# Kernel tuning notes

Hardware: AMD Instinct MI355X
Metric: run time of the kernel (lower is better)

The kernel has to match this reference:

```python
import jax, jax.numpy as jnp
import numpy as np
import math

B, S, D_MODEL, H = 4, 256, 2048, 256
HEAD_DIM = D_MODEL // H  # 8


def setup_inputs() -> dict:
    key = jax.random.key(0)
    ks = jax.random.split(key, 10)
    w_scale = 0.02
    inp = {
        "x": jax.random.normal(ks[0], (B, S, D_MODEL), dtype=jnp.float32),
        "phase_shift": jax.random.normal(ks[1], (H, 1, 1), dtype=jnp.float32),
        "Wq": jax.random.normal(ks[2], (D_MODEL, D_MODEL), dtype=jnp.float32) * w_scale,
        "bq": jnp.zeros((D_MODEL,), dtype=jnp.float32),
        "Wk": jax.random.normal(ks[3], (D_MODEL, D_MODEL), dtype=jnp.float32) * w_scale,
        "bk": jnp.zeros((D_MODEL,), dtype=jnp.float32),
        "Wv": jax.random.normal(ks[4], (D_MODEL, D_MODEL), dtype=jnp.float32) * w_scale,
        "bv": jnp.zeros((D_MODEL,), dtype=jnp.float32),
        "Wo": jax.random.normal(ks[5], (D_MODEL, D_MODEL), dtype=jnp.float32) * w_scale,
        "bo": jnp.zeros((D_MODEL,), dtype=jnp.float32),
    }
    return inp


def _forward(x, phase_shift, Wq, bq, Wk, bk, Wv, bv, Wo, bo):
    b, s, dm = x.shape
    h = phase_shift.shape[0]
    d = dm // h
    # projections (torch Linear with random weights; stored as [in,out])
    q = (x @ Wq + bq).reshape(b, s, h, d)
    k = (x @ Wk + bk).reshape(b, s, h, d)
    v = (x @ Wv + bv).reshape(b, s, h, d)
    # complex phase rotation: q *= exp(+i phi), k *= exp(-i phi)
    # phase_shift (h,1,1) broadcasts against (b,s,h,d) -> varies along the s dim (requires s==h)
    c = jnp.cos(phase_shift)  # (h,1,1)
    sn = jnp.sin(phase_shift)
    qr, qi = q * c, q * sn          # Re/Im of rotated q
    kr, ki = k * c, -(k * sn)       # Re/Im of rotated k
    scale = 1.0 / math.sqrt(d)
    # per-(b,s) head-mixing scores: [b,s,h,h], complex matmul split into real/imag
    sr = (jnp.einsum('bshd,bsgd->bshg', qr, kr)
          - jnp.einsum('bshd,bsgd->bshg', qi, ki)) * scale
    si = (jnp.einsum('bshd,bsgd->bshg', qr, ki)
          + jnp.einsum('bshd,bsgd->bshg', qi, kr)) * scale  # analytically 0 (phases cancel)
    attn_r = jax.nn.softmax(sr, axis=-1)
    attn_i = jax.nn.softmax(si, axis=-1)  # faithful dual softmax; v is real so only
    # Re(attention @ v) = attn_r @ v reaches the output (.real is taken before o_proj)
    del attn_i
    out = jnp.einsum('bshg,bsgd->bshd', attn_r, v).reshape(b, s, dm)
    return out @ Wo + bo


def reference(x, phase_shift, Wq, bq, Wk, bk, Wv, bv, Wo, bo):
    return _forward(x, phase_shift, Wq, bq, Wk, bk, Wv, bv, Wo, bo)
```

## Files before the change

kernel.cpp:

```cpp
#include <hip/hip_runtime.h>
#include <math.h>

#define M_TOK 1024
#define DM    2048
#define NH    256
#define HD    8
#define SCALE 0.35355339059327373f
#define LOG2E 1.4426950408889634f

typedef _Float16 f16x8 __attribute__((ext_vector_type(8)));
typedef _Float16 f16x4 __attribute__((ext_vector_type(4)));
typedef float    f32x4 __attribute__((ext_vector_type(4)));

#if defined(__has_builtin)
#  if __has_builtin(__builtin_amdgcn_exp2f)
#    define EXP2(x) __builtin_amdgcn_exp2f(x)
#  endif
#endif
#ifndef EXP2
#  define EXP2(x) exp2f(x)
#endif

template<int N>
__device__ __forceinline__ void vm_wait() {
    if constexpr (N == 0) asm volatile("s_waitcnt vmcnt(0)" ::: "memory");
    else if constexpr (N == 1) asm volatile("s_waitcnt vmcnt(1)" ::: "memory");
    else if constexpr (N == 2) asm volatile("s_waitcnt vmcnt(2)" ::: "memory");
    else if constexpr (N == 3) asm volatile("s_waitcnt vmcnt(3)" ::: "memory");
    else if constexpr (N == 4) asm volatile("s_waitcnt vmcnt(4)" ::: "memory");
    else if constexpr (N == 5) asm volatile("s_waitcnt vmcnt(5)" ::: "memory");
    else if constexpr (N == 6) asm volatile("s_waitcnt vmcnt(6)" ::: "memory");
    else if constexpr (N == 7) asm volatile("s_waitcnt vmcnt(7)" ::: "memory");
    else static_assert(N <= 7, "add vmcnt case");
}

__device__ __forceinline__ void raw_barrier() {
    asm volatile("" ::: "memory");
    __builtin_amdgcn_s_barrier();
    asm volatile("" ::: "memory");
}

__global__ __launch_bounds__(256) void prep(
    const float* __restrict__ x, _Float16* __restrict__ xh,
    const float* __restrict__ W0, const float* __restrict__ W1,
    const float* __restrict__ W2, const float* __restrict__ W3,
    _Float16* __restrict__ T0, _Float16* __restrict__ T1,
    _Float16* __restrict__ T2, _Float16* __restrict__ T3)
{
    __shared__ float t[64][65];
    const int tid = threadIdx.x;
    const int z   = blockIdx.z;

    if (z == 4) {
        const int i = (blockIdx.y * 32 + blockIdx.x) * 256 + tid;
        const float4 a = ((const float4*)x)[2 * i];
        const float4 b = ((const float4*)x)[2 * i + 1];
        f16x8 v;
        v[0] = (_Float16)a.x; v[1] = (_Float16)a.y; v[2] = (_Float16)a.z; v[3] = (_Float16)a.w;
        v[4] = (_Float16)b.x; v[5] = (_Float16)b.y; v[6] = (_Float16)b.z; v[7] = (_Float16)b.w;
        ((f16x8*)xh)[i] = v;
        return;
    }

    const float* W = (z == 0) ? W0 : (z == 1) ? W1 : (z == 2) ? W2 : W3;
    _Float16*    T = (z == 0) ? T0 : (z == 1) ? T1 : (z == 2) ? T2 : T3;

    const int nb = blockIdx.x * 64;
    const int kb = blockIdx.y * 64;
    const int tr = tid >> 4;
    const int tc = (tid & 15) << 2;

    #pragma unroll
    for (int rr = 0; rr < 4; ++rr) {
        const int k = kb + rr * 16 + tr;
        const float4 v = *(const float4*)&W[(size_t)k * DM + nb + tc];
        t[rr * 16 + tr][tc + 0] = v.x;
        t[rr * 16 + tr][tc + 1] = v.y;
        t[rr * 16 + tr][tc + 2] = v.z;
        t[rr * 16 + tr][tc + 3] = v.w;
    }
    __syncthreads();
    #pragma unroll
    for (int rr = 0; rr < 4; ++rr) {
        const int n = nb + rr * 16 + tr;
        f16x4 v;
        #pragma unroll
        for (int j = 0; j < 4; ++j)
            v[j] = (_Float16)t[tc + j][rr * 16 + tr];
        *(f16x4*)&T[(size_t)n * DM + kb + tc] = v;
    }
}

template<int WGR, int WGC, int WTR, int WTC, bool F16OUT, int CS, bool SPLIT>
__global__ __launch_bounds__(512, 2) void gemm_p3(
    const _Float16* __restrict__ A,
    const _Float16* __restrict__ Bt,
    const float* __restrict__ b0, const float* __restrict__ b1,
    const float* __restrict__ b2, void* __restrict__ C)
{
    constexpr int NW  = WGR * WGC;
    static_assert(NW == 8, "8 waves");
    constexpr int BM  = WGR * WTR * 16;
    constexpr int BN  = WGC * WTC * 16;
    constexpr int NA  = BM / 8;
    constexpr int NB  = BN / 8;
    constexpr int NC  = NA + NB;
    constexpr int CPW = NC / NW;
    static_assert(NC % NW == 0);
    constexpr int S0  = (CPW + 1) / 2;
    constexpr int BUF = (BM + BN) * 64;
    constexpr int KT  = 32;
    static_assert((KT - 2) % 3 == 0 || true);

    __shared__ _Float16 smem[3 * BUF];

    const int bn = blockIdx.x * BN;
    const int bm = blockIdx.y * BM;

    const int tid  = threadIdx.x;
    const int lane = tid & 63;
    const int wv   = tid >> 6;
    const int wr   = (wv / WGC) * (WTR * 16);
    const int wc   = (wv % WGC) * (WTC * 16);
    const int lr   = lane & 15;
    const int lk   = lane >> 4;
    const int rx   = lr & 7;

    const _Float16* gsrc[CPW];
    int             loff[CPW];
    #pragma unroll
    for (int p = 0; p < CPW; ++p) {
        const int c   = wv * CPW + p;
        const int kch = ((lane & 7) ^ (lane >> 3)) << 3;
        if (c < NA) {
            const int rl = c * 8 + (lane >> 3);
            gsrc[p] = A + (size_t)(bm + rl) * DM + kch;
            loff[p] = c * 512 + lane * 8;
        } else {
            const int rl = (c - NA) * 8 + (lane >> 3);
            gsrc[p] = Bt + (size_t)(bn + rl) * DM + kch;
            loff[p] = BM * 64 + (c - NA) * 512 + lane * 8;
        }
    }

    int offA[WTR][2], offB[WTC][2];
    #pragma unroll
    for (int ks = 0; ks < 2; ++ks) {
        const int sw = (((ks << 2) | lk) ^ rx) << 3;
        #pragma unroll
        for (int i = 0; i < WTR; ++i)
            offA[i][ks] = (wr + i * 16 + lr) * 64 + sw;
        #pragma unroll
        for (int j = 0; j < WTC; ++j)
            offB[j][ks] = BM * 64 + (wc + j * 16 + lr) * 64 + sw;
    }

    f32x4 acc[WTR][WTC] = {};

    auto stage = [&](int buf, int from, int to) {
        #pragma unroll
        for (int p = 0; p < CPW; ++p) {
            if (p >= from && p < to) {
                __builtin_amdgcn_global_load_lds(
                    (const __attribute__((address_space(1))) void*)gsrc[p],
                    (__attribute__((address_space(3))) void*)(smem + buf * BUF + loff[p]),
                    16, 0, 0);
                gsrc[p] += 64;
            }
        }
    };

    auto cphase = [&](int buf, int ks) {
        const _Float16* base = smem + buf * BUF;
        f16x8 aF[WTR], bF[WTC];
        #pragma unroll
        for (int i = 0; i < WTR; ++i)
            aF[i] = *(const f16x8*)&base[offA[i][ks]];
        #pragma unroll
        for (int j = 0; j < WTC; ++j)
            bF[j] = *(const f16x8*)&base[offB[j][ks]];
        __builtin_amdgcn_s_setprio(1);
        #pragma unroll
        for (int i = 0; i < WTR; ++i)
            #pragma unroll
            for (int j = 0; j < WTC; ++j)
                acc[i][j] = __builtin_amdgcn_mfma_f32_16x16x32_f16(aF[i], bF[j], acc[i][j], 0, 0, 0);
        __builtin_amdgcn_s_setprio(0);
    };

    auto tile = [&](int buf, bool do_stage, bool last) {
        if (last) vm_wait<0>();
        else      vm_wait<CPW>();
        raw_barrier();
        const int nb3 = (buf + 2 >= 3) ? buf - 1 : buf + 2;
        if (do_stage) stage(nb3, 0, S0);
        cphase(buf, 0);
        if (SPLIT) raw_barrier();
        if (do_stage) stage(nb3, S0, CPW);
        cphase(buf, 1);
        raw_barrier();
    };

    stage(0, 0, CPW);
    stage(1, 0, CPW);
    #pragma unroll 1
    for (int tt = 0; tt < KT - 2; tt += 3) {
        tile(0, true, false);
        tile(1, true, false);
        tile(2, true, false);
    }
    tile(0, false, false);
    tile(1, false, true);

    #pragma unroll
    for (int i = 0; i < WTR; ++i) {
        #pragma unroll
        for (int j = 0; j < WTC; ++j) {
            const int col = bn + wc + j * 16 + lr;
            float bv;
            if constexpr (CS > DM) {
                const float* bp = (col < 2048) ? b0 : (col < 4096) ? b1 : b2;
                bv = bp[col & 2047];
            } else {
                bv = b0[col];
            }
            #pragma unroll
            for (int r = 0; r < 4; ++r) {
                const int row = bm + wr + i * 16 + lk * 4 + r;
                const float v = acc[i][j][r] + bv;
                if (F16OUT)
                    ((_Float16*)C)[(size_t)row * CS + col] = (_Float16)v;
                else
                    ((float*)C)[(size_t)row * CS + col] = v;
            }
        }
    }
}

__global__ __launch_bounds__(256) void attn_mfma(
    const _Float16* __restrict__ QKV, _Float16* __restrict__ Oh)
{
    __shared__ _Float16 Vt[8][264];
    __shared__ _Float16 Al[256][72];
    __shared__ _Float16 Ot[256][8];

    const int tid  = threadIdx.x;
    const int lane = tid & 63;
    const int wv   = tid >> 6;
    const int col  = lane & 15;
    const int quad = lane >> 4;
    const int hbase = wv * 64;

    #pragma unroll 1
    for (int tt = 0; tt < 2; ++tt) {
        const int t = blockIdx.x * 2 + tt;
        const _Float16* qb = QKV + (size_t)t * (3 * DM);
        const _Float16* kb = qb + DM;
        const _Float16* vb = qb + 2 * DM;

        __syncthreads();

        {
            const f16x8 v = *(const f16x8*)(vb + tid * 8);
            #pragma unroll
            for (int d = 0; d < 8; ++d) Vt[d][tid] = v[d];
        }

        f16x8 qf[4];
        #pragma unroll
        for (int ht = 0; ht < 4; ++ht) {
            f16x8 v = {};
            if (quad == 0)
                v = *(const f16x8*)(qb + (hbase + ht * 16 + col) * 8);
            #pragma unroll
            for (int j = 0; j < 8; ++j) qf[ht][j] = v[j] * (_Float16)(SCALE * LOG2E);
        }

        __syncthreads();

        const f32x4 zf = {};
        float rsum[4] = {};
        f32x4 oacc[4] = {};

        #pragma unroll 1
        for (int c = 0; c < 4; ++c) {
            const int gchunk = c * 64;

            f16x8 kf[4];
            #pragma unroll
            for (int gt = 0; gt < 4; ++gt) {
                f16x8 v = {};
                if (quad == 0)
                    v = *(const f16x8*)(kb + (gchunk + gt * 16 + col) * 8);
                kf[gt] = v;
            }

            f32x4 s[4][4];
            #pragma unroll
            for (int gt = 0; gt < 4; ++gt)
                #pragma unroll
                for (int ht = 0; ht < 4; ++ht)
                    s[gt][ht] = __builtin_amdgcn_mfma_f32_16x16x32_f16(kf[gt], qf[ht], zf, 0, 0, 0);

            #pragma unroll
            for (int gt = 0; gt < 4; ++gt) {
                #pragma unroll
                for (int ht = 0; ht < 4; ++ht) {
                    f16x4 e4;
                    #pragma unroll
                    for (int r = 0; r < 4; ++r) {
                        e4[r] = (_Float16)EXP2(s[gt][ht][r]);
                        rsum[ht] += (float)e4[r];
                    }
                    *(f16x4*)&Al[hbase + ht * 16 + col][gt * 16 + quad * 4] = e4;
                }
            }

            #pragma unroll
            for (int ks = 0; ks < 2; ++ks) {
                f16x8 vf = {};
                if (col < 8)
                    vf = *(const f16x8*)&Vt[col][gchunk + ks * 32 + quad * 8];
                #pragma unroll
                for (int ht = 0; ht < 4; ++ht) {
                    const f16x8 af = *(const f16x8*)&Al[hbase + ht * 16 + col][ks * 32 + quad * 8];
                    oacc[ht] = __builtin_amdgcn_mfma_f32_16x16x32_f16(af, vf, oacc[ht], 0, 0, 0);
                }
            }
        }

        #pragma unroll
        for (int ht = 0; ht < 4; ++ht) {
            rsum[ht] += __shfl_xor(rsum[ht], 16, 64);
            rsum[ht] += __shfl_xor(rsum[ht], 32, 64);
        }

        #pragma unroll
        for (int ht = 0; ht < 4; ++ht) {
            #pragma unroll
            for (int r = 0; r < 4; ++r) {
                const float sh = __shfl(rsum[ht], quad * 4 + r, 64);
                const float v  = oacc[ht][r] / sh;
                if (col < 8)
                    Ot[hbase + ht * 16 + quad * 4 + r][col] = (_Float16)v;
            }
        }
        const f16x8 ov = *(const f16x8*)&Ot[tid][0];
        *(f16x8*)(Oh + (size_t)t * DM + tid * 8) = ov;
    }
}

extern "C" void kernel_launch(void* const* d_in, const int* in_sizes, int n_in,
                              void* d_out, int out_size, void* d_ws, size_t ws_size,
                              hipStream_t stream)
{
    const float* x  = (const float*)d_in[0];
    const float* Wq = (const float*)d_in[2];
    const float* bq = (const float*)d_in[3];
    const float* Wk = (const float*)d_in[4];
    const float* bk = (const float*)d_in[5];
    const float* Wv = (const float*)d_in[6];
    const float* bv = (const float*)d_in[7];
    const float* Wo = (const float*)d_in[8];
    const float* bo = (const float*)d_in[9];
    float* out = (float*)d_out;

    char* ws = (char*)d_ws;
    _Float16* xh  = (_Float16*)(ws);
    _Float16* Wt  = (_Float16*)(ws + (4u  << 20));
    _Float16* Wto = (_Float16*)(ws + (28u << 20));
    _Float16* QKV = (_Float16*)(ws + (36u << 20));
    _Float16* Oh  = (_Float16*)(ws + (48u << 20));

    prep<<<dim3(32, 32, 5), dim3(256), 0, stream>>>(
        x, xh, Wq, Wk, Wv, Wo,
        Wt, Wt + 2048 * 2048, Wt + 2 * 2048 * 2048, Wto);

    gemm_p3<2, 4, 4, 3, true, 3 * DM, true><<<dim3(32, 8), dim3(512), 0, stream>>>(
        xh, Wt, bq, bk, bv, (void*)QKV);

    attn_mfma<<<dim3(M_TOK / 2), dim3(256), 0, stream>>>(QKV, Oh);

    gemm_p3<2, 4, 2, 2, false, DM, false><<<dim3(16, 16), dim3(512), 0, stream>>>(
        Oh, Wto, bo, bo, bo, (void*)out);
}
```

Baseline: 185.2 us.

## Parameterize GEMM pipeline depth; use four LDS buffers for output projection

Templates the GEMM on the number of LDS buffers, adding a 4-buffer variant with prefetch depth 3. The output-projection GEMM uses it to keep more global loads in flight. Async global-to-LDS staging now issues after the fragment reads inside each compute phase, not before them. The extra buffer raises LDS use per block, which may limit occupancy, and the hand-written vmcnt waits must match the staging counts exactly.

```diff
diff --git a/kernel.cpp b/kernel.cpp
--- a/kernel.cpp
+++ b/kernel.cpp
@@ -31,7 +31,8 @@
     else if constexpr (N == 5) asm volatile("s_waitcnt vmcnt(5)" ::: "memory");
     else if constexpr (N == 6) asm volatile("s_waitcnt vmcnt(6)" ::: "memory");
     else if constexpr (N == 7) asm volatile("s_waitcnt vmcnt(7)" ::: "memory");
-    else static_assert(N <= 7, "add vmcnt case");
+    else if constexpr (N == 8) asm volatile("s_waitcnt vmcnt(8)" ::: "memory");
+    else static_assert(N <= 8, "add vmcnt case");
 }
 
 __device__ __forceinline__ void raw_barrier() {
@@ -91,7 +92,7 @@
     }
 }
 
-template<int WGR, int WGC, int WTR, int WTC, bool F16OUT, int CS, bool SPLIT>
+template<int WGR, int WGC, int WTR, int WTC, bool F16OUT, int CS, bool SPLIT, int NBUF>
 __global__ __launch_bounds__(512, 2) void gemm_p3(
     const _Float16* __restrict__ A,
     const _Float16* __restrict__ Bt,
@@ -100,6 +101,7 @@
 {
     constexpr int NW  = WGR * WGC;
     static_assert(NW == 8, "8 waves");
+    constexpr int D   = NBUF - 1;
     constexpr int BM  = WGR * WTR * 16;
     constexpr int BN  = WGC * WTC * 16;
     constexpr int NA  = BM / 8;
@@ -110,9 +112,9 @@
     constexpr int S0  = (CPW + 1) / 2;
     constexpr int BUF = (BM + BN) * 64;
     constexpr int KT  = 32;
-    static_assert((KT - 2) % 3 == 0 || true);
-
-    __shared__ _Float16 smem[3 * BUF];
+    constexpr int WMAIN = (D - 1) * CPW;
+
+    __shared__ _Float16 smem[NBUF * BUF];
 
     const int bn = blockIdx.x * BN;
     const int bm = blockIdx.y * BM;
@@ -157,20 +159,20 @@
 
     f32x4 acc[WTR][WTC] = {};
 
-    auto stage = [&](int buf, int from, int to) {
+    auto stage = [&](int sbuf, int from, int to) {
         #pragma unroll
         for (int p = 0; p < CPW; ++p) {
             if (p >= from && p < to) {
                 __builtin_amdgcn_global_load_lds(
                     (const __attribute__((address_space(1))) void*)gsrc[p],
-                    (__attribute__((address_space(3))) void*)(smem + buf * BUF + loff[p]),
+                    (__attribute__((address_space(3))) void*)(smem + sbuf * BUF + loff[p]),
                     16, 0, 0);
                 gsrc[p] += 64;
             }
         }
     };
 
-    auto cphase = [&](int buf, int ks) {
+    auto phase = [&](int buf, int ks, int sbuf, int from, int to, bool do_stage) {
         const _Float16* base = smem + buf * BUF;
         f16x8 aF[WTR], bF[WTC];
         #pragma unroll
@@ -179,6 +181,7 @@
         #pragma unroll
         for (int j = 0; j < WTC; ++j)
             bF[j] = *(const f16x8*)&base[offB[j][ks]];
+        if (do_stage) stage(sbuf, from, to);
         __builtin_amdgcn_s_setprio(1);
         #pragma unroll
         for (int i = 0; i < WTR; ++i)
@@ -188,29 +191,39 @@
         __builtin_amdgcn_s_setprio(0);
     };
 
-    auto tile = [&](int buf, bool do_stage, bool last) {
-        if (last) vm_wait<0>();
-        else      vm_wait<CPW>();
+    auto tile = [&](int buf, int sbuf, bool do_stage) {
         raw_barrier();
-        const int nb3 = (buf + 2 >= 3) ? buf - 1 : buf + 2;
-        if (do_stage) stage(nb3, 0, S0);
-        cphase(buf, 0);
+        phase(buf, 0, sbuf, 0, S0, do_stage);
         if (SPLIT) raw_barrier();
-        if (do_stage) stage(nb3, S0, CPW);
-        cphase(buf, 1);
+        phase(buf, 1, sbuf, S0, CPW, do_stage);
         raw_barrier();
     };
 
-    stage(0, 0, CPW);
-    stage(1, 0, CPW);
-    #pragma unroll 1
-    for (int tt = 0; tt < KT - 2; tt += 3) {
-        tile(0, true, false);
-        tile(1, true, false);
-        tile(2, true, false);
-    }
-    tile(0, false, false);
-    tile(1, false, true);
+    if constexpr (NBUF == 3) {
+        stage(0, 0, CPW); stage(1, 0, CPW);
+        #pragma unroll 1
+        for (int tt = 0; tt < KT - 2; tt += 3) {
+            vm_wait<WMAIN>(); tile(0, 2, true);
+            vm_wait<WMAIN>(); tile(1, 0, true);
+            vm_wait<WMAIN>(); tile(2, 1, true);
+        }
+        vm_wait<WMAIN>(); tile(0, 0, false);
+        vm_wait<0>();     tile(1, 0, false);
+    } else {
+        static_assert(NBUF == 4);
+        stage(0, 0, CPW); stage(1, 0, CPW); stage(2, 0, CPW);
+        #pragma unroll 1
+        for (int tt = 0; tt < KT - 4; tt += 4) {
+            vm_wait<WMAIN>(); tile(0, 3, true);
+            vm_wait<WMAIN>(); tile(1, 0, true);
+            vm_wait<WMAIN>(); tile(2, 1, true);
+            vm_wait<WMAIN>(); tile(3, 2, true);
+        }
+        vm_wait<WMAIN>(); tile(0, 3, true);
+        vm_wait<WMAIN>(); tile(1, 0, false);
+        vm_wait<CPW>();   tile(2, 0, false);
+        vm_wait<0>();     tile(3, 0, false);
+    }
 
     #pragma unroll
     for (int i = 0; i < WTR; ++i) {
@@ -376,11 +389,11 @@
         x, xh, Wq, Wk, Wv, Wo,
         Wt, Wt + 2048 * 2048, Wt + 2 * 2048 * 2048, Wto);
 
-    gemm_p3<2, 4, 4, 3, true, 3 * DM, true><<<dim3(32, 8), dim3(512), 0, stream>>>(
+    gemm_p3<2, 4, 4, 3, true, 3 * DM, true, 3><<<dim3(32, 8), dim3(512), 0, stream>>>(
         xh, Wt, bq, bk, bv, (void*)QKV);
 
     attn_mfma<<<dim3(M_TOK / 2), dim3(256), 0, stream>>>(QKV, Oh);
 
-    gemm_p3<2, 4, 2, 2, false, DM, false><<<dim3(16, 16), dim3(512), 0, stream>>>(
+    gemm_p3<2, 4, 2, 2, false, DM, false, 4><<<dim3(16, 16), dim3(512), 0, stream>>>(
         Oh, Wto, bo, bo, bo, (void*)out);
 }
```

New measurement: 186.3 us, median of 2. About the same (+0.6%).
